# Performance work log

Measured on AMD Instinct MI355X. Metric: run time of the kernel, lower is better.

Reference implementation:

```python
import jax, jax.numpy as jnp
import numpy as np

NCLASSES = 80
MAX_BOXES = 100
IOU_THR = 0.5
SCORE_THR = 0.0
NEG = -1e9


def arrange_bbox(xy, wh):
    # xy, wh: [1, H, W, 3, 2]
    H, W = xy.shape[1], xy.shape[2]
    gx, gy = jnp.meshgrid(jnp.arange(W), jnp.arange(H))  # 'xy' indexing, each [H, W]
    grid = jnp.stack([gx, gy], axis=-1)[:, :, None, :].astype(xy.dtype)  # [H, W, 1, 2]
    gsize = jnp.array([H, W], dtype=xy.dtype)  # TF divides last dim [x, y] by [H, W]
    xy = (xy + grid) / gsize
    return jnp.concatenate([xy - wh / 2, xy + wh / 2], axis=-1)  # [1,H,W,3,4]


def hard_nms(boxes, scores):
    # boxes: [N,4] (x1,y1,x2,y2); scores: [N]. Greedy NMS, fixed MAX_BOXES output.
    areas = (boxes[:, 2] - boxes[:, 0]) * (boxes[:, 3] - boxes[:, 1])  # [N]

    def step(sw, _):
        j = jnp.argmax(sw)
        s = sw[j]
        valid = s > SCORE_THR
        bj = boxes[j]
        iw = jnp.clip(jnp.minimum(boxes[:, 2], bj[2]) - jnp.maximum(boxes[:, 0], bj[0]), 0.0)
        ih = jnp.clip(jnp.minimum(boxes[:, 3], bj[3]) - jnp.maximum(boxes[:, 1], bj[1]), 0.0)
        inter = iw * ih
        iou = inter / (areas + areas[j] - inter)
        sw = jnp.where((iou > IOU_THR) & valid, NEG, sw)  # suppresses j itself too
        return sw, (jnp.where(valid, j, -1), jnp.where(valid, s, 0.0), valid)

    _, (sel_idx, sel_scores, valids) = jax.lax.scan(step, scores, None, length=MAX_BOXES)
    return sel_idx, sel_scores, valids


def decode(grid0, grid1, grid2, anchors_table):
    outs = (grid0, grid1, grid2)
    anch = (anchors_table[2], anchors_table[1], anchors_table[0])
    bbs, confs, probs = [], [], []
    for g, a in zip(outs, anch):
        xy, wh, obj, cp = jnp.split(g, [2, 4, 5], axis=-1)
        b = arrange_bbox(xy, jnp.exp(wh) * a)
        bbs.append(b.reshape(1, -1, 4))
        confs.append(obj.reshape(1, -1, 1))
        probs.append(cp.reshape(1, -1, NCLASSES))
    bbox = jnp.concatenate(bbs, axis=1).reshape(-1, 4)          # [N,4]
    conf = jnp.concatenate(confs, axis=1)[0, :, 0]              # [N]
    cp = jnp.concatenate(probs, axis=1)[0]                      # [N,C]
    cls_idx = jnp.argmax(cp, axis=-1)                           # [N]
    maxprob = jnp.max(cp, axis=-1)                              # [N]
    # TF code broadcasts conf[1,N,1]*maxprob[N] -> [N,N], then reduce_max over axis 1.
    # Mathematically: scores[i] = max_j conf[i]*maxprob[j] = max(conf*max(mp), conf*min(mp)).
    scores = jnp.maximum(conf * jnp.max(maxprob), conf * jnp.min(maxprob))
    return bbox, scores, cls_idx


def reference(grid0, grid1, grid2, anchors_table):
    bbox, scores, cls_idx = decode(grid0, grid1, grid2, anchors_table)
    sel_idx, sel_scores, valids = hard_nms(bbox, scores)
    safe = jnp.clip(sel_idx, 0)
    sel_boxes = jnp.where(valids[:, None], bbox[safe], 0.0)[None]      # [1,MAX,4]
    sel_scores = sel_scores[None]                                       # [1,MAX]
    sel_classes = jnp.where(valids, cls_idx[safe], 0)[None]            # [1,MAX]
    num_valid = jnp.sum(valids).astype(jnp.int32)[None]                # [1]
    return sel_boxes, sel_scores, sel_classes, num_valid


def setup_inputs() -> dict:
    key = jax.random.key(0)
    k0, k1, k2 = jax.random.split(key, 3)
    grid0 = jax.random.normal(k0, (1, 48, 48, 3, 85), jnp.float32)
    grid1 = jax.random.normal(k1, (1, 96, 96, 3, 85), jnp.float32)
    grid2 = jax.random.normal(k2, (1, 192, 192, 3, 85), jnp.float32)
    anchors = np.array([[[10, 13], [16, 30], [33, 23]],
                        [[30, 61], [62, 45], [59, 119]],
                        [[116, 90], [156, 198], [373, 326]]], np.float32) / 416.0
    return {"grid0": grid0, "grid1": grid1, "grid2": grid2,
            "anchors_table": jnp.asarray(anchors)}
```

## Files before the change

### kernel.cpp

```cpp
#include <hip/hip_runtime.h>
#include <hip/hip_bf16.h>
#include <math.h>


#define NCLS  80
#define MAXB  100
#define N0    6912
#define N1    27648
#define NTOT  145152
#define NTILE 2268
#define NB    4096
#define CAP   2048
#define CAPL  2048
#define CHUNK 256
#define NEGF  -3.402823466e38f
#define POSF   3.402823466e38f

#define WS_CONF 0
#define WS_SCAL (NTOT * 4)
#define WS_PART (WS_SCAL + 16)
#define WS_HIST (WS_PART + NTILE * 16)
#define WS_BINC (WS_HIST + 8 * NB * 4)
#define WS_SUF  (WS_BINC + NB * 4)
#define WS_META (WS_SUF + (NB + 2) * 4)
#define WS_CAND (WS_META + 16)

__device__ __forceinline__ int binOf(float s, float Smax) {
    int b = (int)((s / Smax) * (float)NB);
    return b > (NB - 1) ? (NB - 1) : b;
}
__device__ __forceinline__ float smaxOf(const float* scal) {
    float Mx = scal[0], Mn = scal[1], cmx = scal[2], cmn = scal[3];
    return fmaxf(fmaxf(cmx * Mx, cmx * Mn), fmaxf(cmn * Mx, cmn * Mn));
}
__device__ __forceinline__ float rdlane(float v, int l) {
    return __uint_as_float(__builtin_amdgcn_readlane(__float_as_uint(v), l));
}
__device__ __forceinline__ void decodeBox(int idx, const float* __restrict__ g0,
        const float* __restrict__ g1, const float* __restrict__ g2,
        const float* __restrict__ anch,
        float& x1, float& y1, float& x2, float& y2) {
    const float* g; int H, ar, j;
    if (idx < N0)           { g = g0; H = 48;  ar = 2; j = idx; }
    else if (idx < N0 + N1) { g = g1; H = 96;  ar = 1; j = idx - N0; }
    else                    { g = g2; H = 192; ar = 0; j = idx - N0 - N1; }
    const float* r = g + (size_t)j * 85;
    float tx = r[0], ty = r[1], tw = r[2], th = r[3];
    int cell = j / 3, a = j - cell * 3;
    int hh = cell / H, ww = cell - hh * H;
    float xc = (tx + (float)ww) / (float)H;
    float yc = (ty + (float)hh) / (float)H;
    float bw = expf(tw) * anch[ar * 6 + a * 2];
    float bh = expf(th) * anch[ar * 6 + a * 2 + 1];
    x1 = xc - bw * 0.5f; y1 = yc - bh * 0.5f;
    x2 = xc + bw * 0.5f; y2 = yc + bh * 0.5f;
}

__global__ __launch_bounds__(256) void k_decode(
        const float* __restrict__ g0, const float* __restrict__ g1,
        const float* __restrict__ g2, float* __restrict__ conf,
        float* __restrict__ part, int* __restrict__ hz) {
    __shared__ float sm[5440];
    __shared__ float red[16];
    const int tid = threadIdx.x;
    const int tile = blockIdx.x;
    {
        int z = tile * 256 + tid;
        if (z < 9 * NB) hz[z] = 0;
    }
    const float* p; int ibase, lt;
    if (tile < 108)      { p = g0; ibase = 0;       lt = tile; }
    else if (tile < 540) { p = g1; ibase = N0;      lt = tile - 108; }
    else                 { p = g2; ibase = N0 + N1; lt = tile - 540; }
    const float4* src = (const float4*)(p + (size_t)lt * 5440);
    for (int w = tid; w < 1360; w += 256) ((float4*)sm)[w] = src[w];
    __syncthreads();

    const int b = tid >> 2, pp = tid & 3;
    const float* row = sm + b * 85;
    float best = row[5 + pp * 20];
    #pragma unroll
    for (int k = 1; k < 20; k++) best = fmaxf(best, row[5 + pp * 20 + k]);
    best = fmaxf(best, __shfl_xor(best, 1));
    best = fmaxf(best, __shfl_xor(best, 2));
    float cmx = NEGF, cmn = POSF;
    if (pp == 0) {
        float obj = row[4];
        conf[ibase + lt * 64 + b] = obj;
        cmx = obj; cmn = obj;
    }
    float mpmax = best, mpmin = best;
    for (int off = 32; off; off >>= 1) {
        mpmax = fmaxf(mpmax, __shfl_down(mpmax, off));
        mpmin = fminf(mpmin, __shfl_down(mpmin, off));
        cmx   = fmaxf(cmx,   __shfl_down(cmx,   off));
        cmn   = fminf(cmn,   __shfl_down(cmn,   off));
    }
    const int lane = tid & 63, wid = tid >> 6;
    if (lane == 0) {
        red[wid * 4 + 0] = mpmax; red[wid * 4 + 1] = mpmin;
        red[wid * 4 + 2] = cmx;   red[wid * 4 + 3] = cmn;
    }
    __syncthreads();
    if (tid == 0) {
        float a0 = red[0], a1 = red[1], a2 = red[2], a3 = red[3];
        for (int w = 1; w < 4; w++) {
            a0 = fmaxf(a0, red[w * 4 + 0]); a1 = fminf(a1, red[w * 4 + 1]);
            a2 = fmaxf(a2, red[w * 4 + 2]); a3 = fminf(a3, red[w * 4 + 3]);
        }
        part[tile * 4 + 0] = a0; part[tile * 4 + 1] = a1;
        part[tile * 4 + 2] = a2; part[tile * 4 + 3] = a3;
    }
}

__global__ __launch_bounds__(256) void k_reduce(const float* __restrict__ part,
                                                float* __restrict__ scal) {
    __shared__ float red[16];
    const int tid = threadIdx.x;
    float a0 = NEGF, a1 = POSF, a2 = NEGF, a3 = POSF;
    for (int b = tid; b < NTILE; b += 256) {
        float4 p4 = ((const float4*)part)[b];
        a0 = fmaxf(a0, p4.x); a1 = fminf(a1, p4.y);
        a2 = fmaxf(a2, p4.z); a3 = fminf(a3, p4.w);
    }
    for (int off = 32; off; off >>= 1) {
        a0 = fmaxf(a0, __shfl_down(a0, off)); a1 = fminf(a1, __shfl_down(a1, off));
        a2 = fmaxf(a2, __shfl_down(a2, off)); a3 = fminf(a3, __shfl_down(a3, off));
    }
    const int lane = tid & 63, wid = tid >> 6;
    if (lane == 0) {
        red[wid * 4 + 0] = a0; red[wid * 4 + 1] = a1;
        red[wid * 4 + 2] = a2; red[wid * 4 + 3] = a3;
    }
    __syncthreads();
    if (tid == 0) {
        for (int w = 1; w < 4; w++) {
            a0 = fmaxf(a0, red[w * 4 + 0]); a1 = fminf(a1, red[w * 4 + 1]);
            a2 = fmaxf(a2, red[w * 4 + 2]); a3 = fminf(a3, red[w * 4 + 3]);
        }
        scal[0] = a0; scal[1] = a1; scal[2] = a2; scal[3] = a3;
    }
}

__global__ __launch_bounds__(256) void k_hist(const float* __restrict__ conf,
                                              const float* __restrict__ scal,
                                              int* __restrict__ hist) {
    int i = blockIdx.x * 256 + threadIdx.x;
    float Mx = scal[0], Mn = scal[1];
    float Smax = smaxOf(scal);
    float c = conf[i];
    float s = fmaxf(c * Mx, c * Mn);
    if (s > 0.0f && Smax > 0.0f)
        atomicAdd(&hist[((blockIdx.x & 7) << 12) + binOf(s, Smax)], 1);
}

__global__ __launch_bounds__(1024) void k_thresh(const int* __restrict__ hist,
                                                 int* __restrict__ suf,
                                                 int* __restrict__ meta) {
    __shared__ int grp[1024];
    const int tid = threadIdx.x;
    int b0 = tid * 4;
    int h[4];
    #pragma unroll
    for (int q = 0; q < 4; q++) {
        int s = 0;
        #pragma unroll
        for (int sh = 0; sh < 8; sh++) s += hist[sh * NB + b0 + q];
        h[q] = s;
    }
    grp[tid] = h[0] + h[1] + h[2] + h[3];
    __syncthreads();
    for (int d = 1; d < 1024; d <<= 1) {
        int add = (tid + d < 1024) ? grp[tid + d] : 0;
        __syncthreads();
        grp[tid] += add;
        __syncthreads();
    }
    int gnext = (tid + 1 < 1024) ? grp[tid + 1] : 0;
    suf[b0 + 3] = gnext + h[3];
    suf[b0 + 2] = gnext + h[3] + h[2];
    suf[b0 + 1] = gnext + h[3] + h[2] + h[1];
    suf[b0 + 0] = gnext + h[3] + h[2] + h[1] + h[0];
    if (tid == 0) suf[NB] = 0;
    __syncthreads();
    if (tid == 0) {
        int L = 0, R = NB - 1, res = NB - 1;
        while (L <= R) {
            int m = (L + R) >> 1;
            if (suf[m] <= CAP) { res = m; R = m - 1; } else L = m + 1;
        }
        meta[0] = res;
    }
}

__global__ __launch_bounds__(256) void k_compact(
        const float* __restrict__ conf, const float* __restrict__ scal,
        const int* __restrict__ suf, const int* __restrict__ meta,
        int* __restrict__ binCtr, unsigned long long* __restrict__ cand) {
    int i = blockIdx.x * 256 + threadIdx.x;
    float Mx = scal[0], Mn = scal[1];
    float Smax = smaxOf(scal);
    float c = conf[i];
    float s = fmaxf(c * Mx, c * Mn);
    int lo = meta[0];
    if (s > 0.0f && Smax > 0.0f) {
        int b = binOf(s, Smax);
        if (b >= lo) {
            int pos = suf[b + 1] + atomicAdd(&binCtr[b], 1);
            if (pos < CAP)
                cand[pos] = ((unsigned long long)__float_as_uint(s) << 32)
                          | (unsigned long long)(~(unsigned)i);
        }
    }
}

__global__ __launch_bounds__(64) void k_nms(
        const float* __restrict__ g0, const float* __restrict__ g1,
        const float* __restrict__ g2, const float* __restrict__ anch,
        const float* __restrict__ conf, const float* __restrict__ scal,
        const int* __restrict__ suf, const int* __restrict__ meta,
        const unsigned long long* __restrict__ cand, float* __restrict__ out) {
    __shared__ unsigned long long keys[CAPL];
    __shared__ float selX1[MAXB], selY1[MAXB], selX2[MAXB], selY2[MAXB],
                     selA[MAXB], selS[MAXB];
    __shared__ int selIdx[MAXB];
    __shared__ int sh_cnt;

    const int lane = threadIdx.x;
    const float Mx = scal[0], Mn = scal[1];
    const float Smax = smaxOf(scal);
    const int loGlob = meta[0];
    int nsel = 0;
    int hi = NB;

    while (nsel < MAXB && hi > 0) {
        const bool fast = hi > loGlob;
        const int sufHi = suf[hi];
        int l;
        {
            int lb = fast ? loGlob : 0;
            int capHere = fast ? CHUNK : CAPL;
            int L = lb, R = hi - 1, res = hi - 1;
            while (L <= R) {
                int m = (L + R) >> 1;
                if (suf[m] - sufHi <= capHere) { res = m; R = m - 1; } else L = m + 1;
            }
            l = res;
        }
        int cnt;
        if (fast) {
            cnt = suf[l] - sufHi;
            for (int i = lane; i < cnt; i += 64) keys[i] = cand[sufHi + i];
        } else {
            if (lane == 0) sh_cnt = 0;
            __syncthreads();
            for (int i = lane; i < NTOT; i += 64) {
                float c = conf[i];
                float s = fmaxf(c * Mx, c * Mn);
                if (s > 0.0f) {
                    int b = binOf(s, Smax);
                    if (b >= l && b < hi) {
                        int pos = atomicAdd(&sh_cnt, 1);
                        if (pos < CAPL)
                            keys[pos] = ((unsigned long long)__float_as_uint(s) << 32)
                                      | (unsigned long long)(~(unsigned)i);
                    }
                }
            }
            __syncthreads();
            cnt = sh_cnt; if (cnt > CAPL) cnt = CAPL;
        }
        if (cnt > 0) {
            if (cnt <= 256) {
                __syncthreads();
                const int t0 = lane * 4;
                unsigned long long mk0 = 0, mk1 = 0, mk2 = 0, mk3 = 0;
                if (t0 + 0 < cnt) mk0 = keys[t0 + 0];
                if (t0 + 1 < cnt) mk1 = keys[t0 + 1];
                if (t0 + 2 < cnt) mk2 = keys[t0 + 2];
                if (t0 + 3 < cnt) mk3 = keys[t0 + 3];
                int r0 = 0, r1 = 0, r2 = 0, r3 = 0;
                #pragma unroll 4
                for (int j = 0; j < cnt; j++) {
                    unsigned long long kj = keys[j];
                    r0 += (kj > mk0) ? 1 : 0; r1 += (kj > mk1) ? 1 : 0;
                    r2 += (kj > mk2) ? 1 : 0; r3 += (kj > mk3) ? 1 : 0;
                }
                __syncthreads();
                if (t0 + 0 < cnt) keys[r0] = mk0;
                if (t0 + 1 < cnt) keys[r1] = mk1;
                if (t0 + 2 < cnt) keys[r2] = mk2;
                if (t0 + 3 < cnt) keys[r3] = mk3;
                __syncthreads();
            } else {
                int n = 2; while (n < cnt) n <<= 1;
                for (int i = cnt + lane; i < n; i += 64) keys[i] = 0ULL;
                __syncthreads();
                for (int k = 2; k <= n; k <<= 1) {
                    for (int j = k >> 1; j > 0; j >>= 1) {
                        int half = n >> 1;
                        for (int t = lane; t < half; t += 64) {
                            int i = ((t & ~(j - 1)) << 1) | (t & (j - 1));
                            int ixj = i | j;
                            unsigned long long ka = keys[i], kb = keys[ixj];
                            if ((ka < kb) == ((i & k) == 0)) { keys[i] = kb; keys[ixj] = ka; }
                        }
                        __syncthreads();
                    }
                }
            }
            for (int bpos = 0; bpos < cnt && nsel < MAXB; bpos += 64) {
                int t = bpos + lane;
                bool alive = (t < cnt);
                float x1 = 0.f, y1 = 0.f, x2 = 0.f, y2 = 0.f, area = 0.f, sc = 0.f;
                int idx = 0;
                if (alive) {
                    unsigned long long key = keys[t];
                    idx = (int)(~(unsigned)key);
                    sc = __uint_as_float((unsigned)(key >> 32));
                    decodeBox(idx, g0, g1, g2, anch, x1, y1, x2, y2);
                    area = (x2 - x1) * (y2 - y1);
                    for (int s2 = 0; s2 < nsel; s2++) {
                        float iw = fminf(x2, selX2[s2]) - fmaxf(x1, selX1[s2]);
                        float ih = fminf(y2, selY2[s2]) - fmaxf(y1, selY1[s2]);
                        iw = fmaxf(iw, 0.f); ih = fmaxf(ih, 0.f);
                        float inter = iw * ih;
                        if (inter / (area + selA[s2] - inter) > 0.5f) { alive = false; break; }
                    }
                }
                while (nsel < MAXB) {
                    unsigned long long bal = __ballot(alive);
                    if (!bal) break;
                    int w = __ffsll((unsigned long long)bal) - 1;
                    float wx1 = rdlane(x1, w), wy1 = rdlane(y1, w);
                    float wx2 = rdlane(x2, w), wy2 = rdlane(y2, w);
                    float wa  = rdlane(area, w);
                    if (lane == w) {
                        selX1[nsel] = x1; selY1[nsel] = y1;
                        selX2[nsel] = x2; selY2[nsel] = y2;
                        selA[nsel] = area; selS[nsel] = sc; selIdx[nsel] = idx;
                    }
                    if (alive) {
                        float iw = fminf(x2, wx2) - fmaxf(x1, wx1);
                        float ih = fminf(y2, wy2) - fmaxf(y1, wy1);
                        iw = fmaxf(iw, 0.f); ih = fmaxf(ih, 0.f);
                        float inter = iw * ih;
                        if (inter / (area + wa - inter) > 0.5f) alive = false;
                    }
                    nsel++;
                }
                __syncthreads();
            }
        }
        hi = l;
    }
    __syncthreads();

    for (int k = lane; k < MAXB; k += 64) {
        float b0 = 0.f, b1 = 0.f, b2 = 0.f, b3 = 0.f, sv = 0.f, cv = 0.f;
        if (k < nsel) {
            b0 = selX1[k]; b1 = selY1[k]; b2 = selX2[k]; b3 = selY2[k];
            sv = selS[k];
            int idx = selIdx[k];
            const float* g; int j;
            if (idx < N0)           { g = g0; j = idx; }
            else if (idx < N0 + N1) { g = g1; j = idx - N0; }
            else                    { g = g2; j = idx - N0 - N1; }
            const float* r = g + (size_t)j * 85 + 5;
            float v[NCLS];
            #pragma unroll
            for (int q = 0; q < NCLS; q++) v[q] = r[q];
            float best = v[0]; int c = 0;
            #pragma unroll
            for (int q = 1; q < NCLS; q++)
                if (v[q] > best) { best = v[q]; c = q; }
            cv = (float)c;
        }
        out[4 * k + 0] = b0; out[4 * k + 1] = b1;
        out[4 * k + 2] = b2; out[4 * k + 3] = b3;
        out[400 + k] = sv;
        out[500 + k] = cv;
    }
    if (lane == 0) out[600] = (float)nsel;
}

extern "C" void kernel_launch(void* const* d_in, const int* in_sizes, int n_in,
                              void* d_out, int out_size, void* d_ws, size_t ws_size,
                              hipStream_t stream) {
    const float* g0   = (const float*)d_in[0];
    const float* g1   = (const float*)d_in[1];
    const float* g2   = (const float*)d_in[2];
    const float* anch = (const float*)d_in[3];
    char* ws = (char*)d_ws;
    float* conf  = (float*)(ws + WS_CONF);
    float* scal  = (float*)(ws + WS_SCAL);
    float* part  = (float*)(ws + WS_PART);
    int*   hist  = (int*)(ws + WS_HIST);
    int*   binc  = (int*)(ws + WS_BINC);
    int*   suf   = (int*)(ws + WS_SUF);
    int*   meta  = (int*)(ws + WS_META);
    unsigned long long* cand = (unsigned long long*)(ws + WS_CAND);
    float* out   = (float*)d_out;

    k_decode <<<NTILE, 256, 0, stream>>>(g0, g1, g2, conf, part, hist);
    k_reduce <<<1, 256, 0, stream>>>(part, scal);
    k_hist   <<<NTOT / 256, 256, 0, stream>>>(conf, scal, hist);
    k_thresh <<<1, 1024, 0, stream>>>(hist, suf, meta);
    k_compact<<<NTOT / 256, 256, 0, stream>>>(conf, scal, suf, meta, binc, cand);
    k_nms    <<<1, 64, 0, stream>>>(g0, g1, g2, anch, conf, scal, suf, meta, cand, out);
}
```

Baseline: 158.0 us.

## Fuse reduce, histogram, threshold and compaction into one single-block kernel

Replaces four kernel launches (reduce, histogram, threshold scan, compaction) with one 1024-thread single-block kernel. The histogram and bin counters move to shared memory, and the decode kernel no longer zeroes global buffers. This removes three launch gaps and the global atomics. In exchange, two full passes over the 145k conf values now run on a single workgroup instead of hundreds of blocks, which may be slower in raw throughput.

```diff
diff --git a/kernel.cpp b/kernel.cpp
--- a/kernel.cpp
+++ b/kernel.cpp
@@ -19,9 +19,7 @@
 #define WS_CONF 0
 #define WS_SCAL (NTOT * 4)
 #define WS_PART (WS_SCAL + 16)
-#define WS_HIST (WS_PART + NTILE * 16)
-#define WS_BINC (WS_HIST + 8 * NB * 4)
-#define WS_SUF  (WS_BINC + NB * 4)
+#define WS_SUF  (WS_PART + NTILE * 16)
 #define WS_META (WS_SUF + (NB + 2) * 4)
 #define WS_CAND (WS_META + 16)
 
@@ -59,15 +57,11 @@
 __global__ __launch_bounds__(256) void k_decode(
         const float* __restrict__ g0, const float* __restrict__ g1,
         const float* __restrict__ g2, float* __restrict__ conf,
-        float* __restrict__ part, int* __restrict__ hz) {
+        float* __restrict__ part) {
     __shared__ float sm[5440];
     __shared__ float red[16];
     const int tid = threadIdx.x;
     const int tile = blockIdx.x;
-    {
-        int z = tile * 256 + tid;
-        if (z < 9 * NB) hz[z] = 0;
-    }
     const float* p; int ibase, lt;
     if (tile < 108)      { p = g0; ibase = 0;       lt = tile; }
     else if (tile < 540) { p = g1; ibase = N0;      lt = tile - 108; }
@@ -113,12 +107,25 @@
     }
 }
 
-__global__ __launch_bounds__(256) void k_reduce(const float* __restrict__ part,
-                                                float* __restrict__ scal) {
-    __shared__ float red[16];
+__global__ __launch_bounds__(1024) void k_mid(
+        const float* __restrict__ part, const float* __restrict__ conf,
+        float* __restrict__ scal, int* __restrict__ suf,
+        int* __restrict__ meta, unsigned long long* __restrict__ cand) {
+    __shared__ int   s_hist[NB];
+    __shared__ int   s_binc[NB];
+    __shared__ int   s_suf[NB + 2];
+    __shared__ int   grp[1024];
+    __shared__ float red[64];
+    __shared__ float s_scal[4];
+    __shared__ int   s_lo;
     const int tid = threadIdx.x;
+    const int lane = tid & 63, wid = tid >> 6;
+
+    #pragma unroll
+    for (int q = 0; q < 4; q++) { s_hist[tid * 4 + q] = 0; s_binc[tid * 4 + q] = 0; }
+
     float a0 = NEGF, a1 = POSF, a2 = NEGF, a3 = POSF;
-    for (int b = tid; b < NTILE; b += 256) {
+    for (int b = tid; b < NTILE; b += 1024) {
         float4 p4 = ((const float4*)part)[b];
         a0 = fmaxf(a0, p4.x); a1 = fminf(a1, p4.y);
         a2 = fmaxf(a2, p4.z); a3 = fminf(a3, p4.w);
@@ -127,89 +134,87 @@
         a0 = fmaxf(a0, __shfl_down(a0, off)); a1 = fminf(a1, __shfl_down(a1, off));
         a2 = fmaxf(a2, __shfl_down(a2, off)); a3 = fminf(a3, __shfl_down(a3, off));
     }
-    const int lane = tid & 63, wid = tid >> 6;
     if (lane == 0) {
         red[wid * 4 + 0] = a0; red[wid * 4 + 1] = a1;
         red[wid * 4 + 2] = a2; red[wid * 4 + 3] = a3;
     }
     __syncthreads();
     if (tid == 0) {
-        for (int w = 1; w < 4; w++) {
+        for (int w = 1; w < 16; w++) {
             a0 = fmaxf(a0, red[w * 4 + 0]); a1 = fminf(a1, red[w * 4 + 1]);
             a2 = fmaxf(a2, red[w * 4 + 2]); a3 = fminf(a3, red[w * 4 + 3]);
         }
+        s_scal[0] = a0; s_scal[1] = a1; s_scal[2] = a2; s_scal[3] = a3;
         scal[0] = a0; scal[1] = a1; scal[2] = a2; scal[3] = a3;
     }
-}
-
-__global__ __launch_bounds__(256) void k_hist(const float* __restrict__ conf,
-                                              const float* __restrict__ scal,
-                                              int* __restrict__ hist) {
-    int i = blockIdx.x * 256 + threadIdx.x;
-    float Mx = scal[0], Mn = scal[1];
-    float Smax = smaxOf(scal);
-    float c = conf[i];
-    float s = fmaxf(c * Mx, c * Mn);
-    if (s > 0.0f && Smax > 0.0f)
-        atomicAdd(&hist[((blockIdx.x & 7) << 12) + binOf(s, Smax)], 1);
-}
-
-__global__ __launch_bounds__(1024) void k_thresh(const int* __restrict__ hist,
-                                                 int* __restrict__ suf,
-                                                 int* __restrict__ meta) {
-    __shared__ int grp[1024];
-    const int tid = threadIdx.x;
-    int b0 = tid * 4;
-    int h[4];
-    #pragma unroll
-    for (int q = 0; q < 4; q++) {
-        int s = 0;
+    __syncthreads();
+
+    const float Mx = s_scal[0], Mn = s_scal[1];
+    const float Smax = smaxOf(s_scal);
+
+    for (int i4 = tid; i4 < NTOT / 4; i4 += 1024) {
+        float4 c4 = ((const float4*)conf)[i4];
+        float cc[4] = {c4.x, c4.y, c4.z, c4.w};
         #pragma unroll
-        for (int sh = 0; sh < 8; sh++) s += hist[sh * NB + b0 + q];
-        h[q] = s;
-    }
-    grp[tid] = h[0] + h[1] + h[2] + h[3];
-    __syncthreads();
-    for (int d = 1; d < 1024; d <<= 1) {
-        int add = (tid + d < 1024) ? grp[tid + d] : 0;
+        for (int q = 0; q < 4; q++) {
+            float s = fmaxf(cc[q] * Mx, cc[q] * Mn);
+            if (s > 0.0f && Smax > 0.0f) atomicAdd(&s_hist[binOf(s, Smax)], 1);
+        }
+    }
+    __syncthreads();
+
+    {
+        int b0 = tid * 4;
+        int h[4];
+        #pragma unroll
+        for (int q = 0; q < 4; q++) h[q] = s_hist[b0 + q];
+        grp[tid] = h[0] + h[1] + h[2] + h[3];
         __syncthreads();
-        grp[tid] += add;
+        for (int d = 1; d < 1024; d <<= 1) {
+            int add = (tid + d < 1024) ? grp[tid + d] : 0;
+            __syncthreads();
+            grp[tid] += add;
+            __syncthreads();
+        }
+        int gnext = (tid + 1 < 1024) ? grp[tid + 1] : 0;
+        int v3 = gnext + h[3];
+        int v2 = v3 + h[2];
+        int v1 = v2 + h[1];
+        int v0 = v1 + h[0];
+        s_suf[b0 + 3] = v3; suf[b0 + 3] = v3;
+        s_suf[b0 + 2] = v2; suf[b0 + 2] = v2;
+        s_suf[b0 + 1] = v1; suf[b0 + 1] = v1;
+        s_suf[b0 + 0] = v0; suf[b0 + 0] = v0;
+        if (tid == 0) { s_suf[NB] = 0; suf[NB] = 0; }
         __syncthreads();
-    }
-    int gnext = (tid + 1 < 1024) ? grp[tid + 1] : 0;
-    suf[b0 + 3] = gnext + h[3];
-    suf[b0 + 2] = gnext + h[3] + h[2];
-    suf[b0 + 1] = gnext + h[3] + h[2] + h[1];
-    suf[b0 + 0] = gnext + h[3] + h[2] + h[1] + h[0];
-    if (tid == 0) suf[NB] = 0;
-    __syncthreads();
-    if (tid == 0) {
-        int L = 0, R = NB - 1, res = NB - 1;
-        while (L <= R) {
-            int m = (L + R) >> 1;
-            if (suf[m] <= CAP) { res = m; R = m - 1; } else L = m + 1;
-        }
-        meta[0] = res;
-    }
-}
-
-__global__ __launch_bounds__(256) void k_compact(
-        const float* __restrict__ conf, const float* __restrict__ scal,
-        const int* __restrict__ suf, const int* __restrict__ meta,
-        int* __restrict__ binCtr, unsigned long long* __restrict__ cand) {
-    int i = blockIdx.x * 256 + threadIdx.x;
-    float Mx = scal[0], Mn = scal[1];
-    float Smax = smaxOf(scal);
-    float c = conf[i];
-    float s = fmaxf(c * Mx, c * Mn);
-    int lo = meta[0];
-    if (s > 0.0f && Smax > 0.0f) {
-        int b = binOf(s, Smax);
-        if (b >= lo) {
-            int pos = suf[b + 1] + atomicAdd(&binCtr[b], 1);
-            if (pos < CAP)
-                cand[pos] = ((unsigned long long)__float_as_uint(s) << 32)
-                          | (unsigned long long)(~(unsigned)i);
+        if (tid == 0) {
+            int L = 0, R = NB - 1, res = NB - 1;
+            while (L <= R) {
+                int m = (L + R) >> 1;
+                if (s_suf[m] <= CAP) { res = m; R = m - 1; } else L = m + 1;
+            }
+            meta[0] = res; s_lo = res;
+        }
+    }
+    __syncthreads();
+
+    const int lo = s_lo;
+    for (int i4 = tid; i4 < NTOT / 4; i4 += 1024) {
+        float4 c4 = ((const float4*)conf)[i4];
+        float cc[4] = {c4.x, c4.y, c4.z, c4.w};
+        #pragma unroll
+        for (int q = 0; q < 4; q++) {
+            int i = i4 * 4 + q;
+            float s = fmaxf(cc[q] * Mx, cc[q] * Mn);
+            if (s > 0.0f && Smax > 0.0f) {
+                int b = binOf(s, Smax);
+                if (b >= lo) {
+                    int pos = s_suf[b + 1] + atomicAdd(&s_binc[b], 1);
+                    if (pos < CAP)
+                        cand[pos] = ((unsigned long long)__float_as_uint(s) << 32)
+                                  | (unsigned long long)(~(unsigned)i);
+                }
+            }
         }
     }
 }
@@ -395,17 +400,12 @@
     float* conf  = (float*)(ws + WS_CONF);
     float* scal  = (float*)(ws + WS_SCAL);
     float* part  = (float*)(ws + WS_PART);
-    int*   hist  = (int*)(ws + WS_HIST);
-    int*   binc  = (int*)(ws + WS_BINC);
     int*   suf   = (int*)(ws + WS_SUF);
     int*   meta  = (int*)(ws + WS_META);
     unsigned long long* cand = (unsigned long long*)(ws + WS_CAND);
     float* out   = (float*)d_out;
 
-    k_decode <<<NTILE, 256, 0, stream>>>(g0, g1, g2, conf, part, hist);
-    k_reduce <<<1, 256, 0, stream>>>(part, scal);
-    k_hist   <<<NTOT / 256, 256, 0, stream>>>(conf, scal, hist);
-    k_thresh <<<1, 1024, 0, stream>>>(hist, suf, meta);
-    k_compact<<<NTOT / 256, 256, 0, stream>>>(conf, scal, suf, meta, binc, cand);
+    k_decode <<<NTILE, 256, 0, stream>>>(g0, g1, g2, conf, part);
+    k_mid    <<<1, 1024, 0, stream>>>(part, conf, scal, suf, meta, cand);
     k_nms    <<<1, 64, 0, stream>>>(g0, g1, g2, anch, conf, scal, suf, meta, cand, out);
 }
```

Measured after the change: 188.4 us. 19.2% more time.

## Process 256 NMS candidates per wave pass with 4 per lane and float4 selected boxes

Applied to the files above, without the earlier changes.

The single-wave NMS loop now gives each lane four candidates, so one pass covers 256 sorted keys instead of 64. The check against already-selected boxes is unrolled by 8 and reads boxes as one float4 from LDS. Each greedy pick is broadcast via readlane, including slot selection, and lane 0 writes it. This cuts loop iterations, syncs and LDS loads in the serial NMS stage, at the cost of more registers per lane and select chains to pick the winning slot.

```diff
diff --git a/kernel.cpp b/kernel.cpp
--- a/kernel.cpp
+++ b/kernel.cpp
@@ -35,6 +35,15 @@
 }
 __device__ __forceinline__ float rdlane(float v, int l) {
     return __uint_as_float(__builtin_amdgcn_readlane(__float_as_uint(v), l));
+}
+__device__ __forceinline__ int rdlanei(int v, int l) {
+    return __builtin_amdgcn_readlane(v, l);
+}
+__device__ __forceinline__ float self4(int s, float a0, float a1, float a2, float a3) {
+    return s == 0 ? a0 : (s == 1 ? a1 : (s == 2 ? a2 : a3));
+}
+__device__ __forceinline__ int seli4(int s, int a0, int a1, int a2, int a3) {
+    return s == 0 ? a0 : (s == 1 ? a1 : (s == 2 ? a2 : a3));
 }
 __device__ __forceinline__ void decodeBox(int idx, const float* __restrict__ g0,
         const float* __restrict__ g1, const float* __restrict__ g2,
@@ -221,8 +230,8 @@
         const int* __restrict__ suf, const int* __restrict__ meta,
         const unsigned long long* __restrict__ cand, float* __restrict__ out) {
     __shared__ unsigned long long keys[CAPL];
-    __shared__ float selX1[MAXB], selY1[MAXB], selX2[MAXB], selY2[MAXB],
-                     selA[MAXB], selS[MAXB];
+    __shared__ float4 selB[MAXB];
+    __shared__ float selA[MAXB], selS[MAXB];
     __shared__ int selIdx[MAXB];
     __shared__ int sh_cnt;
 
@@ -309,43 +318,80 @@
                     }
                 }
             }
-            for (int bpos = 0; bpos < cnt && nsel < MAXB; bpos += 64) {
-                int t = bpos + lane;
-                bool alive = (t < cnt);
-                float x1 = 0.f, y1 = 0.f, x2 = 0.f, y2 = 0.f, area = 0.f, sc = 0.f;
-                int idx = 0;
-                if (alive) {
-                    unsigned long long key = keys[t];
-                    idx = (int)(~(unsigned)key);
-                    sc = __uint_as_float((unsigned)(key >> 32));
-                    decodeBox(idx, g0, g1, g2, anch, x1, y1, x2, y2);
-                    area = (x2 - x1) * (y2 - y1);
-                    for (int s2 = 0; s2 < nsel; s2++) {
-                        float iw = fminf(x2, selX2[s2]) - fmaxf(x1, selX1[s2]);
-                        float ih = fminf(y2, selY2[s2]) - fmaxf(y1, selY1[s2]);
+            for (int t0 = 0; t0 < cnt && nsel < MAXB; t0 += 256) {
+                float cx1[4], cy1[4], cx2[4], cy2[4], car[4], csc[4];
+                int cid[4], am = 0;
+                #pragma unroll
+                for (int q = 0; q < 4; q++) {
+                    int ci = t0 + lane * 4 + q;
+                    cx1[q] = 0.f; cy1[q] = 0.f; cx2[q] = 0.f; cy2[q] = 0.f;
+                    car[q] = 0.f; csc[q] = 0.f; cid[q] = 0;
+                    if (ci < cnt) {
+                        unsigned long long key = keys[ci];
+                        cid[q] = (int)(~(unsigned)key);
+                        csc[q] = __uint_as_float((unsigned)(key >> 32));
+                        decodeBox(cid[q], g0, g1, g2, anch,
+                                  cx1[q], cy1[q], cx2[q], cy2[q]);
+                        car[q] = (cx2[q] - cx1[q]) * (cy2[q] - cy1[q]);
+                        am |= 1 << q;
+                    }
+                }
+                if (nsel > 0) {
+                    #pragma unroll
+                    for (int q = 0; q < 4; q++) {
+                        if (!(am & (1 << q))) continue;
+                        bool dead = false;
+                        int s2 = 0;
+                        for (; s2 + 8 <= nsel; s2 += 8) {
+                            #pragma unroll
+                            for (int u = 0; u < 8; u++) {
+                                float4 sb = selB[s2 + u];
+                                float sa = selA[s2 + u];
+                                float iw = fminf(cx2[q], sb.z) - fmaxf(cx1[q], sb.x);
+                                float ih = fminf(cy2[q], sb.w) - fmaxf(cy1[q], sb.y);
+                                iw = fmaxf(iw, 0.f); ih = fmaxf(ih, 0.f);
+                                float inter = iw * ih;
+                                dead = dead | (inter / (car[q] + sa - inter) > 0.5f);
+                            }
+                            if (dead) break;
+                        }
+                        if (!dead) {
+                            for (; s2 < nsel; s2++) {
+                                float4 sb = selB[s2];
+                                float sa = selA[s2];
+                                float iw = fminf(cx2[q], sb.z) - fmaxf(cx1[q], sb.x);
+                                float ih = fminf(cy2[q], sb.w) - fmaxf(cy1[q], sb.y);
+                                iw = fmaxf(iw, 0.f); ih = fmaxf(ih, 0.f);
+                                float inter = iw * ih;
+                                if (inter / (car[q] + sa - inter) > 0.5f) { dead = true; break; }
+                            }
+                        }
+                        if (dead) am &= ~(1 << q);
+                    }
+                }
+                while (nsel < MAXB) {
+                    unsigned long long bal = __ballot(am != 0);
+                    if (!bal) break;
+                    int w = __ffsll(bal) - 1;
+                    int slot = __ffs(rdlanei(am, w)) - 1;
+                    float wx1 = rdlane(self4(slot, cx1[0], cx1[1], cx1[2], cx1[3]), w);
+                    float wy1 = rdlane(self4(slot, cy1[0], cy1[1], cy1[2], cy1[3]), w);
+                    float wx2 = rdlane(self4(slot, cx2[0], cx2[1], cx2[2], cx2[3]), w);
+                    float wy2 = rdlane(self4(slot, cy2[0], cy2[1], cy2[2], cy2[3]), w);
+                    float wa  = rdlane(self4(slot, car[0], car[1], car[2], car[3]), w);
+                    float ws  = rdlane(self4(slot, csc[0], csc[1], csc[2], csc[3]), w);
+                    int   wi  = rdlanei(seli4(slot, cid[0], cid[1], cid[2], cid[3]), w);
+                    if (lane == 0) {
+                        selB[nsel] = make_float4(wx1, wy1, wx2, wy2);
+                        selA[nsel] = wa; selS[nsel] = ws; selIdx[nsel] = wi;
+                    }
+                    #pragma unroll
+                    for (int q = 0; q < 4; q++) {
+                        float iw = fminf(cx2[q], wx2) - fmaxf(cx1[q], wx1);
+                        float ih = fminf(cy2[q], wy2) - fmaxf(cy1[q], wy1);
                         iw = fmaxf(iw, 0.f); ih = fmaxf(ih, 0.f);
                         float inter = iw * ih;
-                        if (inter / (area + selA[s2] - inter) > 0.5f) { alive = false; break; }
-                    }
-                }
-                while (nsel < MAXB) {
-                    unsigned long long bal = __ballot(alive);
-                    if (!bal) break;
-                    int w = __ffsll((unsigned long long)bal) - 1;
-                    float wx1 = rdlane(x1, w), wy1 = rdlane(y1, w);
-                    float wx2 = rdlane(x2, w), wy2 = rdlane(y2, w);
-                    float wa  = rdlane(area, w);
-                    if (lane == w) {
-                        selX1[nsel] = x1; selY1[nsel] = y1;
-                        selX2[nsel] = x2; selY2[nsel] = y2;
-                        selA[nsel] = area; selS[nsel] = sc; selIdx[nsel] = idx;
-                    }
-                    if (alive) {
-                        float iw = fminf(x2, wx2) - fmaxf(x1, wx1);
-                        float ih = fminf(y2, wy2) - fmaxf(y1, wy1);
-                        iw = fmaxf(iw, 0.f); ih = fmaxf(ih, 0.f);
-                        float inter = iw * ih;
-                        if (inter / (area + wa - inter) > 0.5f) alive = false;
+                        if (inter / (car[q] + wa - inter) > 0.5f) am &= ~(1 << q);
                     }
                     nsel++;
                 }
@@ -359,7 +405,8 @@
     for (int k = lane; k < MAXB; k += 64) {
         float b0 = 0.f, b1 = 0.f, b2 = 0.f, b3 = 0.f, sv = 0.f, cv = 0.f;
         if (k < nsel) {
-            b0 = selX1[k]; b1 = selY1[k]; b2 = selX2[k]; b3 = selY2[k];
+            float4 sb = selB[k];
+            b0 = sb.x; b1 = sb.y; b2 = sb.z; b3 = sb.w;
             sv = selS[k];
             int idx = selIdx[k];
             const float* g; int j;
```

After: 200.5 us. 1.27x slower.

## Compute per-batch IoU bitmask matrix for parallel greedy NMS acceptance

Applied to the files above, without the earlier changes.

Within each 64-candidate batch, every lane computes a 64-bit IoU suppression mask against all batch boxes held in shared memory. Greedy acceptance then runs as a cheap scalar loop of mask ANDs instead of serial ballot/readlane/IoU rounds. The selected-box arrays are also packed into float4 so the check against prior selections needs fewer LDS loads. This adds a 64x64 IoU computation per batch, and a fallback to the old serial path when a lane's self-IoU test fails (e.g. degenerate boxes).

```diff
diff --git a/kernel.cpp b/kernel.cpp
--- a/kernel.cpp
+++ b/kernel.cpp
@@ -35,6 +35,9 @@
 }
 __device__ __forceinline__ float rdlane(float v, int l) {
     return __uint_as_float(__builtin_amdgcn_readlane(__float_as_uint(v), l));
+}
+__device__ __forceinline__ unsigned rdlaneu(unsigned v, int l) {
+    return (unsigned)__builtin_amdgcn_readlane((int)v, l);
 }
 __device__ __forceinline__ void decodeBox(int idx, const float* __restrict__ g0,
         const float* __restrict__ g1, const float* __restrict__ g2,
@@ -221,9 +224,10 @@
         const int* __restrict__ suf, const int* __restrict__ meta,
         const unsigned long long* __restrict__ cand, float* __restrict__ out) {
     __shared__ unsigned long long keys[CAPL];
-    __shared__ float selX1[MAXB], selY1[MAXB], selX2[MAXB], selY2[MAXB],
-                     selA[MAXB], selS[MAXB];
+    __shared__ float4 selB[MAXB];
+    __shared__ float selA[MAXB], selS[MAXB];
     __shared__ int selIdx[MAXB];
+    __shared__ float bX1[64], bY1[64], bX2[64], bY2[64], bA[64];
     __shared__ int sh_cnt;
 
     const int lane = threadIdx.x;
@@ -321,33 +325,78 @@
                     decodeBox(idx, g0, g1, g2, anch, x1, y1, x2, y2);
                     area = (x2 - x1) * (y2 - y1);
                     for (int s2 = 0; s2 < nsel; s2++) {
-                        float iw = fminf(x2, selX2[s2]) - fmaxf(x1, selX1[s2]);
-                        float ih = fminf(y2, selY2[s2]) - fmaxf(y1, selY1[s2]);
+                        float4 sb = selB[s2];
+                        float sa = selA[s2];
+                        float iw = fminf(x2, sb.z) - fmaxf(x1, sb.x);
+                        float ih = fminf(y2, sb.w) - fmaxf(y1, sb.y);
                         iw = fmaxf(iw, 0.f); ih = fmaxf(ih, 0.f);
                         float inter = iw * ih;
-                        if (inter / (area + selA[s2] - inter) > 0.5f) { alive = false; break; }
+                        if (inter / (area + sa - inter) > 0.5f) { alive = false; break; }
                     }
                 }
-                while (nsel < MAXB) {
-                    unsigned long long bal = __ballot(alive);
-                    if (!bal) break;
-                    int w = __ffsll((unsigned long long)bal) - 1;
-                    float wx1 = rdlane(x1, w), wy1 = rdlane(y1, w);
-                    float wx2 = rdlane(x2, w), wy2 = rdlane(y2, w);
-                    float wa  = rdlane(area, w);
-                    if (lane == w) {
-                        selX1[nsel] = x1; selY1[nsel] = y1;
-                        selX2[nsel] = x2; selY2[nsel] = y2;
-                        selA[nsel] = area; selS[nsel] = sc; selIdx[nsel] = idx;
-                    }
-                    if (alive) {
-                        float iw = fminf(x2, wx2) - fmaxf(x1, wx1);
-                        float ih = fminf(y2, wy2) - fmaxf(y1, wy1);
+                unsigned long long aliveM = __ballot(alive);
+                if (aliveM != 0ULL) {
+                    bX1[lane] = x1; bY1[lane] = y1;
+                    bX2[lane] = x2; bY2[lane] = y2; bA[lane] = area;
+                    __syncthreads();
+                    unsigned rlo = 0, rhi = 0;
+                    #pragma unroll 4
+                    for (int i = 0; i < 64; i++) {
+                        float vx1 = bX1[i], vy1 = bY1[i];
+                        float vx2 = bX2[i], vy2 = bY2[i], va = bA[i];
+                        float iw = fminf(vx2, x2) - fmaxf(vx1, x1);
+                        float ih = fminf(vy2, y2) - fmaxf(vy1, y1);
                         iw = fmaxf(iw, 0.f); ih = fmaxf(ih, 0.f);
                         float inter = iw * ih;
-                        if (inter / (area + wa - inter) > 0.5f) alive = false;
+                        bool k = inter / (va + area - inter) > 0.5f;
+                        if (i < 32) rlo |= (k ? 1u : 0u) << i;
+                        else        rhi |= (k ? 1u : 0u) << (i - 32);
                     }
-                    nsel++;
+                    bool diag = (((lane < 32) ? (rlo >> lane)
+                                              : (rhi >> (lane - 32))) & 1u) != 0;
+                    unsigned long long bad = __ballot(alive && !diag);
+                    if (bad == 0ULL) {
+                        unsigned long long am = aliveM, accept = 0ULL;
+                        int room = MAXB - nsel;
+                        while (am != 0ULL && room > 0) {
+                            int i = __ffsll(am) - 1;
+                            accept |= 1ULL << i;
+                            unsigned klo = rdlaneu(rlo, i);
+                            unsigned khi = rdlaneu(rhi, i);
+                            am &= ~(((unsigned long long)khi << 32)
+                                    | (unsigned long long)klo);
+                            room--;
+                        }
+                        if ((accept >> lane) & 1ULL) {
+                            int pos = nsel
+                                + __popcll(accept & ((1ULL << lane) - 1ULL));
+                            selB[pos] = make_float4(x1, y1, x2, y2);
+                            selA[pos] = area; selS[pos] = sc; selIdx[pos] = idx;
+                        }
+                        nsel += __popcll(accept);
+                        if (nsel > MAXB) nsel = MAXB;
+                    } else {
+                        while (nsel < MAXB) {
+                            unsigned long long bal = __ballot(alive);
+                            if (!bal) break;
+                            int w = __ffsll((unsigned long long)bal) - 1;
+                            float wx1 = rdlane(x1, w), wy1 = rdlane(y1, w);
+                            float wx2 = rdlane(x2, w), wy2 = rdlane(y2, w);
+                            float wa  = rdlane(area, w);
+                            if (lane == w) {
+                                selB[nsel] = make_float4(x1, y1, x2, y2);
+                                selA[nsel] = area; selS[nsel] = sc; selIdx[nsel] = idx;
+                            }
+                            if (alive) {
+                                float iw = fminf(x2, wx2) - fmaxf(x1, wx1);
+                                float ih = fminf(y2, wy2) - fmaxf(y1, wy1);
+                                iw = fmaxf(iw, 0.f); ih = fmaxf(ih, 0.f);
+                                float inter = iw * ih;
+                                if (inter / (area + wa - inter) > 0.5f) alive = false;
+                            }
+                            nsel++;
+                        }
+                    }
                 }
                 __syncthreads();
             }
@@ -359,7 +408,8 @@
     for (int k = lane; k < MAXB; k += 64) {
         float b0 = 0.f, b1 = 0.f, b2 = 0.f, b3 = 0.f, sv = 0.f, cv = 0.f;
         if (k < nsel) {
-            b0 = selX1[k]; b1 = selY1[k]; b2 = selX2[k]; b3 = selY2[k];
+            float4 sb = selB[k];
+            b0 = sb.x; b1 = sb.y; b2 = sb.z; b3 = sb.w;
             sv = selS[k];
             int idx = selIdx[k];
             const float* g; int j;
```

New measurement: 152.1 us, median of 2. -3.8%, faster.
